# Optimization experiments

Measured on AMD Instinct MI355X. Metric: run time of the kernel, lower is better.

## Reference

```python
import jax, jax.numpy as jnp
import numpy as np

DIM = 512
NH = 16
HEAD = DIM // NH  # 32
WS1 = 8   # window_size // 2 (shift_h=True)
WS2 = 16  # window_size
SHIFT = 4  # window_size // 4


def _rotary(t, cos, sin):
    # t: (..., C); split even/odd channels, rotate, concat halves
    x1, x2 = t[..., 0::2], t[..., 1::2]
    return jnp.concatenate([x1 * cos - x2 * sin, x2 * cos + x1 * sin], axis=-1)


def setup_inputs() -> dict:
    key = jax.random.key(0)
    ks = jax.random.split(key, 8)
    B, H, W = 8, 64, 64
    G = (H // WS1) * (W // WS2)  # 32
    N = WS1 * WS2                # 128
    s = 1.0 / np.sqrt(DIM)
    return {
        "x": jax.random.normal(ks[0], (B, H, W, DIM), jnp.float32),
        "pos_embed_q": jax.random.normal(ks[1], (2, G, 1, N, HEAD // 2), jnp.float32),
        "pos_embed_kv": jax.random.normal(ks[2], (2, G, 1, 2 * N, HEAD // 2), jnp.float32),
        "mask": jnp.zeros((G, 1, N, 2 * N), jnp.float32),
        "w_q": jax.random.normal(ks[3], (DIM, DIM), jnp.float32) * s,
        "b_q": jnp.zeros((DIM,), jnp.float32),
        "w_kv": jax.random.normal(ks[4], (DIM, 2 * DIM), jnp.float32) * s,
        "b_kv": jnp.zeros((2 * DIM,), jnp.float32),
        "w_proj": jax.random.normal(ks[5], (DIM, DIM), jnp.float32) * s,
        "b_proj": jnp.zeros((DIM,), jnp.float32),
        "H": H,
        "W": W,
    }


def reference(x, pos_embed_q, pos_embed_kv, mask, w_q, b_q, w_kv, b_kv, w_proj, b_proj, H, W):
    B = x.shape[0]
    G = (H // WS1) * (W // WS2)
    N = WS1 * WS2
    C = HEAD

    # q projection + window partition -> (B, G, nH, N, C)
    q = x @ w_q + b_q
    q = q.reshape(B, H // WS1, WS1, W // WS2, WS2, NH, C)
    q = q.transpose(0, 1, 3, 5, 2, 4, 6).reshape(B, G, NH, N, C)

    # kv projection, two opposite rolls along H, window partition -> (2, B, G, nH, 2N, C)
    kv = x @ w_kv + b_kv                              # (B,H,W,2D)
    kvs = jnp.stack([jnp.roll(kv, -SHIFT, axis=1), jnp.roll(kv, SHIFT, axis=1)])  # (2shift,B,H,W,2D)
    kvs = kvs.reshape(2, B, H // WS1, WS1, W // WS2, WS2, 2, NH, C)
    kvs = kvs.transpose(6, 1, 2, 4, 7, 0, 3, 5, 8).reshape(2, B, G, NH, 2 * N, C)
    k, v = kvs[0], kvs[1]

    # rotary position embedding
    q = _rotary(q, pos_embed_q[0], pos_embed_q[1])
    k = _rotary(k, pos_embed_kv[0], pos_embed_kv[1])

    # scaled dot product attention with additive mask (eval: no dropout)
    scale = 1.0 / np.sqrt(C)
    scores = jnp.einsum('bgnqc,bgnkc->bgnqk', q, k) * scale + mask
    attn = jax.nn.softmax(scores, axis=-1)
    o = jnp.einsum('bgnqk,bgnkc->bgnqc', attn, v)     # (B,G,nH,N,C)

    # window un-partition -> (B, H, W, D), output projection
    o = o.reshape(B, H // WS1, W // WS2, NH, WS1, WS2, C)
    o = o.transpose(0, 1, 4, 2, 5, 3, 6).reshape(B, H, W, DIM)
    return o @ w_proj + b_proj
```

## Files before the change

### kernel.cpp

```cpp
#include <hip/hip_runtime.h>

typedef __bf16 bf16x8 __attribute__((ext_vector_type(8)));
typedef __bf16 bf16x4 __attribute__((ext_vector_type(4)));
typedef float f32x4 __attribute__((ext_vector_type(4)));

#define DEV __device__ __forceinline__

DEV f32x4 mfma16(bf16x8 a, bf16x8 b, f32x4 c) {
    return __builtin_amdgcn_mfma_f32_16x16x32_bf16(a, b, c, 0, 0, 0);
}

DEV void async16(const void* g, void* l) {
    __builtin_amdgcn_global_load_lds((__attribute__((address_space(1))) void*)g,
                                     (__attribute__((address_space(3))) void*)l, 16, 0, 0);
}

#define LDS_FENCE() asm volatile("" ::: "memory")

__global__ __launch_bounds__(256) void cast_x_kernel(const float4* __restrict__ in,
                                                     bf16x8* __restrict__ out) {
    int i = blockIdx.x * 256 + threadIdx.x;
    float4 a = in[2 * i], b = in[2 * i + 1];
    bf16x8 o;
    o[0] = (__bf16)a.x; o[1] = (__bf16)a.y; o[2] = (__bf16)a.z; o[3] = (__bf16)a.w;
    o[4] = (__bf16)b.x; o[5] = (__bf16)b.y; o[6] = (__bf16)b.z; o[7] = (__bf16)b.w;
    out[i] = o;
}

__global__ void transpose_cast_kernel(const float* __restrict__ src,
                                      __bf16* __restrict__ dst, int R, int C) {
    __shared__ float tile[32][33];
    int tx = threadIdx.x, ty = threadIdx.y;
    int c0 = blockIdx.x * 32, r0 = blockIdx.y * 32;
#pragma unroll
    for (int j = 0; j < 4; ++j)
        tile[ty + j * 8][tx] = src[(size_t)(r0 + ty + j * 8) * C + c0 + tx];
    __syncthreads();
#pragma unroll
    for (int j = 0; j < 4; ++j)
        dst[(size_t)(c0 + ty + j * 8) * R + r0 + tx] = (__bf16)tile[tx][ty + j * 8];
}

__global__ __launch_bounds__(256) void mask_flag_kernel(const float* __restrict__ mask,
                                                        int* __restrict__ flags) {
    int g = blockIdx.x;
    const float4* m4 = (const float4*)(mask + (size_t)g * 32768);
    int any = 0;
    for (int i = threadIdx.x; i < 8192; i += 256) {
        float4 v = m4[i];
        any |= (v.x != 0.f) | (v.y != 0.f) | (v.z != 0.f) | (v.w != 0.f);
    }
    any = __any(any) ? 1 : 0;
    __shared__ int s;
    if (threadIdx.x == 0) s = 0;
    __syncthreads();
    if ((threadIdx.x & 63) == 0 && any) atomicOr(&s, 1);
    __syncthreads();
    if (threadIdx.x == 0) flags[g] = s;
}

__global__ __launch_bounds__(256) void gemm_bt(const __bf16* __restrict__ A,
                                               const __bf16* __restrict__ Bt,
                                               const float* __restrict__ bias0,
                                               const float* __restrict__ bias1,
                                               void* __restrict__ Cout, int N, int outF32) {
    __shared__ __bf16 As[128 * 64];
    __shared__ __bf16 Bs[128 * 64];
    const int tid = threadIdx.x;
    const int bm = blockIdx.x, bn = blockIdx.y;
    const int lane = tid & 63, wv = tid >> 6;
    const int quad = lane >> 4, l16 = lane & 15;
    const int wm = (wv & 1) * 64, wn = (wv >> 1) * 64;
    const __bf16* Abase = A + (size_t)bm * 128 * 512;
    const __bf16* Bbase = Bt + (size_t)bn * 128 * 512;
    f32x4 acc[4][4] = {};
    for (int kr = 0; kr < 8; ++kr) {
#pragma unroll
        for (int i = 0; i < 4; ++i) {
            int chunk = i * 256 + tid;
            int r = chunk >> 3, cc = chunk & 7;
            async16(Abase + r * 512 + kr * 64 + cc * 8, &As[chunk * 8]);
            async16(Bbase + r * 512 + kr * 64 + cc * 8, &Bs[chunk * 8]);
        }
        __syncthreads();
#pragma unroll
        for (int kk = 0; kk < 2; ++kk) {
            bf16x8 af[4], bfm[4];
#pragma unroll
            for (int t = 0; t < 4; ++t) {
                af[t]  = *(const bf16x8*)&As[(wm + t * 16 + l16) * 64 + kk * 32 + quad * 8];
                bfm[t] = *(const bf16x8*)&Bs[(wn + t * 16 + l16) * 64 + kk * 32 + quad * 8];
            }
#pragma unroll
            for (int mt = 0; mt < 4; ++mt)
#pragma unroll
                for (int nt = 0; nt < 4; ++nt)
                    acc[mt][nt] = mfma16(af[mt], bfm[nt], acc[mt][nt]);
        }
        __syncthreads();
    }
#pragma unroll
    for (int nt = 0; nt < 4; ++nt) {
        int ng = bn * 128 + wn + nt * 16 + l16;
        float bias = (ng < 512) ? bias0[ng] : bias1[ng - 512];
#pragma unroll
        for (int mt = 0; mt < 4; ++mt) {
#pragma unroll
            for (int r = 0; r < 4; ++r) {
                int mg = bm * 128 + wm + mt * 16 + quad * 4 + r;
                float v = acc[mt][nt][r] + bias;
                if (outF32) ((float*)Cout)[(size_t)mg * N + ng] = v;
                else ((__bf16*)Cout)[(size_t)mg * N + ng] = (__bf16)v;
            }
        }
    }
}

#define ATT_SCALE 0.17677669529663687f

__global__ __launch_bounds__(256, 4) void attn_kernel(const __bf16* __restrict__ qkv,
                                                      const float* __restrict__ peq,
                                                      const float* __restrict__ pekv,
                                                      const float* __restrict__ mask,
                                                      const int* __restrict__ mflags,
                                                      __bf16* __restrict__ oatt) {
    __shared__ __align__(16) char smem[38400];
    __bf16* Ks = (__bf16*)smem;
    __bf16* Vt = (__bf16*)(smem + 16384);
    __bf16* Ps = (__bf16*)(smem + 33280);

    const int tid = threadIdx.x;
    const int bid = ((blockIdx.x & 7) << 9) | (blockIdx.x >> 3);
    const int b = bid >> 9;
    const int g = (bid >> 4) & 31;
    const int nh = bid & 15;
    const int gh = g >> 2, gw = g & 3;
    const int lane = tid & 63, wv = tid >> 6;
    const int quad = lane >> 4, l16 = lane & 15;

#pragma unroll
    for (int it = 0; it < 4; ++it) {
        int item = it * 256 + tid;
        int ko = item >> 2, c8 = item & 3;
        int roll = ko >> 7, n = ko & 127;
        int h = (gh * 8 + (n >> 4) + (roll ? 60 : 4)) & 63;
        int w = gw * 16 + (n & 15);
        int row = (b * 64 + h) * 64 + w;
        bf16x8 v = *(const bf16x8*)(qkv + (size_t)row * 1536 + 512 + nh * 32 + c8 * 8);
        int pidx = (g * 256 + ko) * 16 + c8 * 4;
        float4 c4 = *(const float4*)(pekv + pidx);
        float4 s4 = *(const float4*)(pekv + 131072 + pidx);
        float cs[4] = {c4.x, c4.y, c4.z, c4.w}, sn[4] = {s4.x, s4.y, s4.z, s4.w};
        bf16x4 lo, hi;
#pragma unroll
        for (int j = 0; j < 4; ++j) {
            float k0 = (float)v[2 * j], k1 = (float)v[2 * j + 1];
            lo[j] = (__bf16)(k0 * cs[j] - k1 * sn[j]);
            hi[j] = (__bf16)(k1 * cs[j] + k0 * sn[j]);
        }
        int sw = (ko >> 1) & 3;
        int base = ko * 32, off = (c8 & 1) * 4;
        *(bf16x4*)&Ks[base + (((c8 >> 1) ^ sw) << 3) + off]       = lo;
        *(bf16x4*)&Ks[base + (((2 + (c8 >> 1)) ^ sw) << 3) + off] = hi;
    }
#pragma unroll
    for (int it = 0; it < 4; ++it) {
        int ko = tid;
        int roll = ko >> 7, n = ko & 127;
        int h = (gh * 8 + (n >> 4) + (roll ? 60 : 4)) & 63;
        int w = gw * 16 + (n & 15);
        int row = (b * 64 + h) * 64 + w;
        bf16x8 v = *(const bf16x8*)(qkv + (size_t)row * 1536 + 1024 + nh * 32 + it * 8);
#pragma unroll
        for (int j = 0; j < 8; ++j)
            Vt[(it * 8 + j) * 264 + ko] = v[j];
    }

    bf16x8 aq[2];
    {
        const int halfsel = quad & 1;
        const bool hi_half = quad >= 2;
#pragma unroll
        for (int rt = 0; rt < 2; ++rt) {
            int n = wv * 32 + rt * 16 + l16;
            int h = gh * 8 + (n >> 4), w = gw * 16 + (n & 15);
            int row = (b * 64 + h) * 64 + w;
            const __bf16* qp = qkv + (size_t)row * 1536 + nh * 32 + halfsel * 16;
            bf16x8 rA = *(const bf16x8*)qp;
            bf16x8 rB = *(const bf16x8*)(qp + 8);
            int pb = (g * 128 + n) * 16 + halfsel * 8;
            float4 ca = *(const float4*)(peq + pb);
            float4 cb = *(const float4*)(peq + pb + 4);
            float4 sa = *(const float4*)(peq + 65536 + pb);
            float4 sb = *(const float4*)(peq + 65536 + pb + 4);
            float cc[8] = {ca.x, ca.y, ca.z, ca.w, cb.x, cb.y, cb.z, cb.w};
            float ss[8] = {sa.x, sa.y, sa.z, sa.w, sb.x, sb.y, sb.z, sb.w};
#pragma unroll
            for (int j = 0; j < 8; ++j) {
                float q0 = (float)(j < 4 ? rA[2 * j] : rB[2 * (j - 4)]);
                float q1 = (float)(j < 4 ? rA[2 * j + 1] : rB[2 * (j - 4) + 1]);
                float r = hi_half ? (q1 * cc[j] + q0 * ss[j]) : (q0 * cc[j] - q1 * ss[j]);
                aq[rt][j] = (__bf16)(r * ATT_SCALE);
            }
        }
    }
    __syncthreads();

    f32x4 o00 = {}, o01 = {}, o10 = {}, o11 = {};
    f32x4 rs0 = {}, rs1 = {};
    const bool use_mask = mflags[g] != 0;
    const float* mg = mask + (size_t)g * 32768;
    __bf16* Pw = Ps + wv * 640;
    const int arow = l16 * 40 + quad * 8;

#pragma unroll 2
    for (int ch = 0; ch < 8; ++ch) {
        bf16x8 vb0 = *(const bf16x8*)&Vt[l16 * 264 + ch * 32 + quad * 8];
        bf16x8 vb1 = *(const bf16x8*)&Vt[(16 + l16) * 264 + ch * 32 + quad * 8];
        f32x4 z = {0.f, 0.f, 0.f, 0.f};
        int key0 = ch * 32 + l16, key1 = key0 + 16;
        bf16x8 bk0 = *(const bf16x8*)&Ks[key0 * 32 + ((quad ^ ((key0 >> 1) & 3)) << 3)];
        bf16x8 bk1 = *(const bf16x8*)&Ks[key1 * 32 + ((quad ^ ((key1 >> 1) & 3)) << 3)];
        f32x4 s00 = mfma16(aq[0], bk0, z), s01 = mfma16(aq[0], bk1, z);
        f32x4 s10 = mfma16(aq[1], bk0, z), s11 = mfma16(aq[1], bk1, z);

        if (use_mask) {
#pragma unroll
            for (int r = 0; r < 4; ++r) {
                int r0 = (wv * 32 + quad * 4 + r) * 256 + ch * 32 + l16;
                int r1 = (wv * 32 + 16 + quad * 4 + r) * 256 + ch * 32 + l16;
                s00[r] += mg[r0];      s01[r] += mg[r0 + 16];
                s10[r] += mg[r1];      s11[r] += mg[r1 + 16];
            }
        }
#pragma unroll
        for (int r = 0; r < 4; ++r) {
            s00[r] = __expf(s00[r]); s01[r] = __expf(s01[r]);
            s10[r] = __expf(s10[r]); s11[r] = __expf(s11[r]);
            rs0[r] += s00[r] + s01[r];
            rs1[r] += s10[r] + s11[r];
        }
#pragma unroll
        for (int r = 0; r < 4; ++r) {
            Pw[(quad * 4 + r) * 40 + l16]      = (__bf16)s00[r];
            Pw[(quad * 4 + r) * 40 + 16 + l16] = (__bf16)s01[r];
        }
        LDS_FENCE();
        bf16x8 a0 = *(const bf16x8*)&Pw[arow];
        LDS_FENCE();
#pragma unroll
        for (int r = 0; r < 4; ++r) {
            Pw[(quad * 4 + r) * 40 + l16]      = (__bf16)s10[r];
            Pw[(quad * 4 + r) * 40 + 16 + l16] = (__bf16)s11[r];
        }
        LDS_FENCE();
        bf16x8 a1 = *(const bf16x8*)&Pw[arow];
        LDS_FENCE();
        o00 = mfma16(a0, vb0, o00); o01 = mfma16(a0, vb1, o01);
        o10 = mfma16(a1, vb0, o10); o11 = mfma16(a1, vb1, o11);
    }

#pragma unroll
    for (int off = 1; off < 16; off <<= 1) {
#pragma unroll
        for (int r = 0; r < 4; ++r) {
            rs0[r] += __shfl_xor(rs0[r], off);
            rs1[r] += __shfl_xor(rs1[r], off);
        }
    }
#pragma unroll
    for (int r = 0; r < 4; ++r) { rs0[r] = 1.f / rs0[r]; rs1[r] = 1.f / rs1[r]; }

#pragma unroll
    for (int r = 0; r < 4; ++r) {
        {
            int rown = wv * 32 + quad * 4 + r;
            int h = gh * 8 + (rown >> 4), w = gw * 16 + (rown & 15);
            size_t base = ((size_t)(b * 64 + h) * 64 + w) * 512 + nh * 32;
            oatt[base + l16]      = (__bf16)(o00[r] * rs0[r]);
            oatt[base + 16 + l16] = (__bf16)(o01[r] * rs0[r]);
        }
        {
            int rown = wv * 32 + 16 + quad * 4 + r;
            int h = gh * 8 + (rown >> 4), w = gw * 16 + (rown & 15);
            size_t base = ((size_t)(b * 64 + h) * 64 + w) * 512 + nh * 32;
            oatt[base + l16]      = (__bf16)(o10[r] * rs1[r]);
            oatt[base + 16 + l16] = (__bf16)(o11[r] * rs1[r]);
        }
    }
}

extern "C" void kernel_launch(void* const* d_in, const int* in_sizes, int n_in,
                              void* d_out, int out_size, void* d_ws, size_t ws_size,
                              hipStream_t stream) {
    const float* x     = (const float*)d_in[0];
    const float* peq   = (const float*)d_in[1];
    const float* pekv  = (const float*)d_in[2];
    const float* mask  = (const float*)d_in[3];
    const float* wq    = (const float*)d_in[4];
    const float* bq    = (const float*)d_in[5];
    const float* wkv   = (const float*)d_in[6];
    const float* bkv   = (const float*)d_in[7];
    const float* wproj = (const float*)d_in[8];
    const float* bproj = (const float*)d_in[9];
    float* out = (float*)d_out;

    char* ws = (char*)d_ws;
    __bf16* xb    = (__bf16*)(ws);
    __bf16* oatt  = (__bf16*)(ws);
    __bf16* wqkvT = (__bf16*)(ws + 33554432);
    int*    mflag = (int*)(ws + 33554432);
    __bf16* wpT   = (__bf16*)(ws + 35127296);
    __bf16* qkv   = (__bf16*)(ws + 35651584);

    cast_x_kernel<<<8192, 256, 0, stream>>>((const float4*)x, (bf16x8*)xb);
    transpose_cast_kernel<<<dim3(16, 16), dim3(32, 8), 0, stream>>>(wq, wqkvT, 512, 512);
    transpose_cast_kernel<<<dim3(32, 16), dim3(32, 8), 0, stream>>>(wkv, wqkvT + 512 * 512, 512, 1024);
    transpose_cast_kernel<<<dim3(16, 16), dim3(32, 8), 0, stream>>>(wproj, wpT, 512, 512);

    gemm_bt<<<dim3(256, 12), 256, 0, stream>>>(xb, wqkvT, bq, bkv, qkv, 1536, 0);
    mask_flag_kernel<<<32, 256, 0, stream>>>(mask, mflag);
    attn_kernel<<<4096, 256, 0, stream>>>(qkv, peq, pekv, mask, mflag, oatt);
    gemm_bt<<<dim3(256, 4), 256, 0, stream>>>(oatt, wpT, bproj, bproj, out, 512, 1);
}
```

Before: 354.3 us.

## Write QKV head-major from GEMM and XOR-swizzle GEMM LDS tiles

The QKV projection GEMM now writes its bf16 output into separate Q, K and V planes, each laid out per head with contiguous 32-element rows, instead of one interleaved 1536-wide row. The attention kernel reads from those planes, so each head's data for a window sits in a compact region rather than being strided by 3 KB. The GEMM LDS tiles also get an XOR swizzle on the 16-byte chunk index to reduce bank conflicts on the fragment reads. The epilogue stores become scattered 2-byte writes with a 64-byte stride, which may cost more on the GEMM side, and the host launch must pass the matching mode.

```diff
diff --git a/kernel.cpp b/kernel.cpp
--- a/kernel.cpp
+++ b/kernel.cpp
@@ -63,7 +63,7 @@
                                                const __bf16* __restrict__ Bt,
                                                const float* __restrict__ bias0,
                                                const float* __restrict__ bias1,
-                                               void* __restrict__ Cout, int N, int outF32) {
+                                               void* __restrict__ Cout, int N, int mode) {
     __shared__ __bf16 As[128 * 64];
     __shared__ __bf16 Bs[128 * 64];
     const int tid = threadIdx.x;
@@ -79,8 +79,9 @@
         for (int i = 0; i < 4; ++i) {
             int chunk = i * 256 + tid;
             int r = chunk >> 3, cc = chunk & 7;
-            async16(Abase + r * 512 + kr * 64 + cc * 8, &As[chunk * 8]);
-            async16(Bbase + r * 512 + kr * 64 + cc * 8, &Bs[chunk * 8]);
+            int src = cc ^ (r & 7);
+            async16(Abase + r * 512 + kr * 64 + src * 8, &As[chunk * 8]);
+            async16(Bbase + r * 512 + kr * 64 + src * 8, &Bs[chunk * 8]);
         }
         __syncthreads();
 #pragma unroll
@@ -88,8 +89,10 @@
             bf16x8 af[4], bfm[4];
 #pragma unroll
             for (int t = 0; t < 4; ++t) {
-                af[t]  = *(const bf16x8*)&As[(wm + t * 16 + l16) * 64 + kk * 32 + quad * 8];
-                bfm[t] = *(const bf16x8*)&Bs[(wn + t * 16 + l16) * 64 + kk * 32 + quad * 8];
+                int ra = wm + t * 16 + l16, rb = wn + t * 16 + l16;
+                int c = kk * 4 + quad;
+                af[t]  = *(const bf16x8*)&As[ra * 64 + ((c ^ (ra & 7)) << 3)];
+                bfm[t] = *(const bf16x8*)&Bs[rb * 64 + ((c ^ (rb & 7)) << 3)];
             }
 #pragma unroll
             for (int mt = 0; mt < 4; ++mt)
@@ -103,15 +106,24 @@
     for (int nt = 0; nt < 4; ++nt) {
         int ng = bn * 128 + wn + nt * 16 + l16;
         float bias = (ng < 512) ? bias0[ng] : bias1[ng - 512];
-#pragma unroll
-        for (int mt = 0; mt < 4; ++mt) {
-#pragma unroll
-            for (int r = 0; r < 4; ++r) {
-                int mg = bm * 128 + wm + mt * 16 + quad * 4 + r;
-                float v = acc[mt][nt][r] + bias;
-                if (outF32) ((float*)Cout)[(size_t)mg * N + ng] = v;
-                else ((__bf16*)Cout)[(size_t)mg * N + ng] = (__bf16)v;
-            }
+        if (mode == 0) {
+            int type = ng >> 9, nhh = (ng >> 5) & 15, c = ng & 31;
+            __bf16* dst = (__bf16*)Cout + (size_t)type * 16777216 + (size_t)nhh * 1048576 + c;
+#pragma unroll
+            for (int mt = 0; mt < 4; ++mt)
+#pragma unroll
+                for (int r = 0; r < 4; ++r) {
+                    int mg = bm * 128 + wm + mt * 16 + quad * 4 + r;
+                    dst[(size_t)mg * 32] = (__bf16)(acc[mt][nt][r] + bias);
+                }
+        } else {
+#pragma unroll
+            for (int mt = 0; mt < 4; ++mt)
+#pragma unroll
+                for (int r = 0; r < 4; ++r) {
+                    int mg = bm * 128 + wm + mt * 16 + quad * 4 + r;
+                    ((float*)Cout)[(size_t)mg * N + ng] = acc[mt][nt][r] + bias;
+                }
         }
     }
 }
@@ -138,6 +150,10 @@
     const int lane = tid & 63, wv = tid >> 6;
     const int quad = lane >> 4, l16 = lane & 15;
 
+    const __bf16* qq = qkv + (size_t)nh * 1048576;
+    const __bf16* kkp = qkv + 16777216 + (size_t)nh * 1048576;
+    const __bf16* vvp = qkv + 33554432 + (size_t)nh * 1048576;
+
 #pragma unroll
     for (int it = 0; it < 4; ++it) {
         int item = it * 256 + tid;
@@ -146,7 +162,7 @@
         int h = (gh * 8 + (n >> 4) + (roll ? 60 : 4)) & 63;
         int w = gw * 16 + (n & 15);
         int row = (b * 64 + h) * 64 + w;
-        bf16x8 v = *(const bf16x8*)(qkv + (size_t)row * 1536 + 512 + nh * 32 + c8 * 8);
+        bf16x8 v = *(const bf16x8*)(kkp + (size_t)row * 32 + c8 * 8);
         int pidx = (g * 256 + ko) * 16 + c8 * 4;
         float4 c4 = *(const float4*)(pekv + pidx);
         float4 s4 = *(const float4*)(pekv + 131072 + pidx);
@@ -170,7 +186,7 @@
         int h = (gh * 8 + (n >> 4) + (roll ? 60 : 4)) & 63;
         int w = gw * 16 + (n & 15);
         int row = (b * 64 + h) * 64 + w;
-        bf16x8 v = *(const bf16x8*)(qkv + (size_t)row * 1536 + 1024 + nh * 32 + it * 8);
+        bf16x8 v = *(const bf16x8*)(vvp + (size_t)row * 32 + it * 8);
 #pragma unroll
         for (int j = 0; j < 8; ++j)
             Vt[(it * 8 + j) * 264 + ko] = v[j];
@@ -185,7 +201,7 @@
             int n = wv * 32 + rt * 16 + l16;
             int h = gh * 8 + (n >> 4), w = gw * 16 + (n & 15);
             int row = (b * 64 + h) * 64 + w;
-            const __bf16* qp = qkv + (size_t)row * 1536 + nh * 32 + halfsel * 16;
+            const __bf16* qp = qq + (size_t)row * 32 + halfsel * 16;
             bf16x8 rA = *(const bf16x8*)qp;
             bf16x8 rB = *(const bf16x8*)(qp + 8);
             int pb = (g * 128 + n) * 16 + halfsel * 8;
```

Measured after the change: 324.8 us. -8.3%, faster.
